# Kernel optimization log

Hardware: AMD Instinct MI355X
Metric: run time of the kernel (lower is better)

Reference implementation:

```python
import jax, jax.numpy as jnp
import numpy as np

# KroneLinear dims (in_a must equal in_b per the source's matmul contraction)
IN_A = 128
IN_B = 128
OUT_A = 128
OUT_B = 128
N = 4096  # batch


def setup_inputs() -> dict:
    key = jax.random.key(0)
    k1, k2, k3, k4 = jax.random.split(key, 4)
    x = jax.random.normal(k1, (N, IN_A * IN_B), dtype=jnp.float32)
    weight_a = jax.random.normal(k2, (OUT_A, IN_A), dtype=jnp.float32) * 0.05
    weight_b = jax.random.normal(k3, (OUT_B, IN_B), dtype=jnp.float32) * 0.05
    bias = jax.random.normal(k4, (OUT_A * OUT_B,), dtype=jnp.float32) * 0.05
    return {"x": x, "weight_a": weight_a, "weight_b": weight_b, "bias": bias}


def reference(x, weight_a, weight_b, bias):
    # vx: view [-1, in_b, in_a] then permute(0,2,1) -> [N, in_a, in_b]
    vx = x.reshape(-1, IN_B, IN_A).transpose(0, 2, 1)
    # torch.matmul(weight_b, vx): contracts weight_b's in_b with vx's dim-1 (in_a)
    # -> [N, out_b, in_b]
    bvx = jnp.einsum('ok,nkj->noj', weight_b, vx)
    # bvx @ weight_a.T -> [N, out_b, out_a]
    bvxa = jnp.einsum('noj,aj->noa', bvx, weight_a)
    # permute(0,2,1) -> [N, out_a, out_b], flatten, add bias
    y = bvxa.transpose(0, 2, 1).reshape(-1, OUT_A * OUT_B) + bias
    return y
```

## Files before the change

### kernel.cpp

```cpp
#include <hip/hip_runtime.h>

typedef __bf16 bf16x8 __attribute__((ext_vector_type(8)));
typedef float f32x4 __attribute__((ext_vector_type(4)));
typedef unsigned int u32x4 __attribute__((ext_vector_type(4)));
typedef unsigned short u16x4 __attribute__((ext_vector_type(4)));

__device__ __forceinline__ unsigned short f2b(float f) {
  union { float f; unsigned int u; } a; a.f = f;
  unsigned int u = a.u;
  u += 0x7fffu + ((u >> 16) & 1u);
  return (unsigned short)(u >> 16);
}

#define LDW 136

__global__ void prep_weights(const float* __restrict__ wa,
                             const float* __restrict__ wb,
                             unsigned short* __restrict__ owa,
                             unsigned short* __restrict__ owb) {
  int t = blockIdx.x * 256 + threadIdx.x;
  if (t < 16384) {
    int j    = t & 7;
    int lane = (t >> 3) & 63;
    int kk   = (t >> 9) & 3;
    int mp   = t >> 11;
    int quad = lane >> 4, l16 = lane & 15;
    owa[t] = f2b(wa[(mp * 16 + l16) * 128 + kk * 32 + quad * 8 + j]);
  } else {
    int u = t - 16384;
    owb[u] = f2b(wb[u]);
  }
}

__global__ __launch_bounds__(512, 4)
void krone_kernel(const float* __restrict__ x,
                  const unsigned short* __restrict__ waf,
                  const unsigned short* __restrict__ wb,
                  const float* __restrict__ bias,
                  float* __restrict__ out) {
  __shared__ unsigned short Mlds[128 * LDW];

  const int tid  = threadIdx.x;
  const int lane = tid & 63;
  const int w    = tid >> 6;
  const int quad = lane >> 4;
  const int l16  = lane & 15;

  const float* xrow = x + (size_t)blockIdx.x * 16384;
  #pragma unroll
  for (int i = 0; i < 8; ++i) {
    int idx = (i << 9) + tid;
    f32x4 v = *(const f32x4*)(xrow + (idx << 2));
    int r = idx >> 5;
    int c = (idx & 31) << 2;
    u16x4 h;
    h[0] = f2b(v[0]); h[1] = f2b(v[1]); h[2] = f2b(v[2]); h[3] = f2b(v[3]);
    *(u16x4*)&Mlds[r * LDW + c] = h;
  }

  bf16x8 wbf[4];
  {
    const unsigned short* wbr = wb + (w * 16 + l16) * 128 + quad * 8;
    #pragma unroll
    for (int kk = 0; kk < 4; ++kk)
      wbf[kk] = __builtin_bit_cast(bf16x8, *(const u32x4*)(wbr + kk * 32));
  }

  __syncthreads();

  u16x4 ur[8];
  #pragma unroll
  for (int m = 0; m < 8; ++m) {
    f32x4 acc = {0.f, 0.f, 0.f, 0.f};
    const unsigned short* mr = &Mlds[(m * 16 + l16) * LDW + quad * 8];
    #pragma unroll
    for (int kk = 0; kk < 4; ++kk) {
      u32x4 ua = *(const u32x4*)(mr + kk * 32);
      acc = __builtin_amdgcn_mfma_f32_16x16x32_bf16(
              __builtin_bit_cast(bf16x8, ua), wbf[kk], acc, 0, 0, 0);
    }
    u16x4 h;
    h[0] = f2b(acc[0]); h[1] = f2b(acc[1]); h[2] = f2b(acc[2]); h[3] = f2b(acc[3]);
    ur[m] = h;
  }

  __syncthreads();

  #pragma unroll
  for (int m = 0; m < 8; ++m)
    *(u16x4*)&Mlds[(w * 16 + l16) * LDW + m * 16 + quad * 4] = ur[m];

  bf16x8 uf[4];
  {
    const unsigned short* utr = &Mlds[(w * 16 + l16) * LDW + quad * 8];
    #pragma unroll
    for (int kk = 0; kk < 4; ++kk)
      uf[kk] = __builtin_bit_cast(bf16x8, *(const u32x4*)(utr + kk * 32));
  }

  float* orow = out + (size_t)blockIdx.x * 16384;
  const unsigned short* wafl = waf + lane * 8;
  #pragma unroll
  for (int mp = 0; mp < 8; ++mp) {
    f32x4 acc = {0.f, 0.f, 0.f, 0.f};
    #pragma unroll
    for (int kk = 0; kk < 4; ++kk) {
      u32x4 ub = *(const u32x4*)(wafl + (mp * 4 + kk) * 512);
      acc = __builtin_amdgcn_mfma_f32_16x16x32_bf16(
              uf[kk], __builtin_bit_cast(bf16x8, ub), acc, 0, 0, 0);
    }
    int r  = mp * 16 + l16;
    int c0 = w * 16 + quad * 4;
    f32x4 b = *(const f32x4*)(bias + r * 128 + c0);
    f32x4 y = acc + b;
    *(f32x4*)(orow + r * 128 + c0) = y;
  }
}

extern "C" void kernel_launch(void* const* d_in, const int* in_sizes, int n_in,
                              void* d_out, int out_size, void* d_ws, size_t ws_size,
                              hipStream_t stream) {
  const float* x  = (const float*)d_in[0];
  const float* wa = (const float*)d_in[1];
  const float* wb = (const float*)d_in[2];
  const float* bs = (const float*)d_in[3];
  float* out = (float*)d_out;

  unsigned short* wsa = (unsigned short*)d_ws;
  unsigned short* wsb = wsa + 128 * 128;

  int N = in_sizes[0] / 16384;

  prep_weights<<<128, 256, 0, stream>>>(wa, wb, wsa, wsb);
  krone_kernel<<<N, 512, 0, stream>>>(x, wsa, wsb, bs, out);
}
```

Baseline: 475.5 us.

## Process four batch rows per block with register-prefetched input pipeline

```diff
diff --git a/kernel.cpp b/kernel.cpp
--- a/kernel.cpp
+++ b/kernel.cpp
@@ -13,6 +13,7 @@
 }
 
 #define LDW 136
+#define G   4
 
 __global__ void prep_weights(const float* __restrict__ wa,
                              const float* __restrict__ wb,
@@ -37,7 +38,7 @@
                   const unsigned short* __restrict__ waf,
                   const unsigned short* __restrict__ wb,
                   const float* __restrict__ bias,
-                  float* __restrict__ out) {
+                  float* __restrict__ out, int Ntot) {
   __shared__ unsigned short Mlds[128 * LDW];
 
   const int tid  = threadIdx.x;
@@ -45,18 +46,11 @@
   const int w    = tid >> 6;
   const int quad = lane >> 4;
   const int l16  = lane & 15;
+  const int n0   = blockIdx.x * G;
+  const int ns   = (Ntot - n0 < G) ? (Ntot - n0) : G;
 
-  const float* xrow = x + (size_t)blockIdx.x * 16384;
-  #pragma unroll
-  for (int i = 0; i < 8; ++i) {
-    int idx = (i << 9) + tid;
-    f32x4 v = *(const f32x4*)(xrow + (idx << 2));
-    int r = idx >> 5;
-    int c = (idx & 31) << 2;
-    u16x4 h;
-    h[0] = f2b(v[0]); h[1] = f2b(v[1]); h[2] = f2b(v[2]); h[3] = f2b(v[3]);
-    *(u16x4*)&Mlds[r * LDW + c] = h;
-  }
+  const int sr = tid >> 5;
+  const int sc = (tid & 31) << 2;
 
   bf16x8 wbf[4];
   {
@@ -66,54 +60,95 @@
       wbf[kk] = __builtin_bit_cast(bf16x8, *(const u32x4*)(wbr + kk * 32));
   }
 
+  f32x4 R[8];
+  {
+    const float* xr = x + (size_t)n0 * 16384 + (tid << 2);
+    #pragma unroll
+    for (int i = 0; i < 8; ++i)
+      R[i] = *(const f32x4*)(xr + (i << 11));
+  }
+  #pragma unroll
+  for (int i = 0; i < 8; ++i) {
+    u16x4 h;
+    h[0] = f2b(R[i][0]); h[1] = f2b(R[i][1]); h[2] = f2b(R[i][2]); h[3] = f2b(R[i][3]);
+    *(u16x4*)&Mlds[(sr + i * 16) * LDW + sc] = h;
+  }
+  if (1 < ns) {
+    const float* xr = x + (size_t)(n0 + 1) * 16384 + (tid << 2);
+    #pragma unroll
+    for (int i = 0; i < 8; ++i)
+      R[i] = *(const f32x4*)(xr + (i << 11));
+  }
   __syncthreads();
 
-  u16x4 ur[8];
-  #pragma unroll
-  for (int m = 0; m < 8; ++m) {
-    f32x4 acc = {0.f, 0.f, 0.f, 0.f};
-    const unsigned short* mr = &Mlds[(m * 16 + l16) * LDW + quad * 8];
+  #pragma unroll 1
+  for (int s = 0; s < ns; ++s) {
+    const int n = n0 + s;
+
+    u16x4 ur[8];
     #pragma unroll
-    for (int kk = 0; kk < 4; ++kk) {
-      u32x4 ua = *(const u32x4*)(mr + kk * 32);
-      acc = __builtin_amdgcn_mfma_f32_16x16x32_bf16(
-              __builtin_bit_cast(bf16x8, ua), wbf[kk], acc, 0, 0, 0);
+    for (int m = 0; m < 8; ++m) {
+      f32x4 acc = {0.f, 0.f, 0.f, 0.f};
+      const unsigned short* mr = &Mlds[(m * 16 + l16) * LDW + quad * 8];
+      #pragma unroll
+      for (int kk = 0; kk < 4; ++kk) {
+        u32x4 ua = *(const u32x4*)(mr + kk * 32);
+        acc = __builtin_amdgcn_mfma_f32_16x16x32_bf16(
+                __builtin_bit_cast(bf16x8, ua), wbf[kk], acc, 0, 0, 0);
+      }
+      u16x4 h;
+      h[0] = f2b(acc[0]); h[1] = f2b(acc[1]); h[2] = f2b(acc[2]); h[3] = f2b(acc[3]);
+      ur[m] = h;
     }
-    u16x4 h;
-    h[0] = f2b(acc[0]); h[1] = f2b(acc[1]); h[2] = f2b(acc[2]); h[3] = f2b(acc[3]);
-    ur[m] = h;
-  }
 
-  __syncthreads();
+    __syncthreads();
 
-  #pragma unroll
-  for (int m = 0; m < 8; ++m)
-    *(u16x4*)&Mlds[(w * 16 + l16) * LDW + m * 16 + quad * 4] = ur[m];
+    #pragma unroll
+    for (int m = 0; m < 8; ++m)
+      *(u16x4*)&Mlds[(w * 16 + l16) * LDW + m * 16 + quad * 4] = ur[m];
+    bf16x8 uf[4];
+    {
+      const unsigned short* utr = &Mlds[(w * 16 + l16) * LDW + quad * 8];
+      #pragma unroll
+      for (int kk = 0; kk < 4; ++kk)
+        uf[kk] = __builtin_bit_cast(bf16x8, *(const u32x4*)(utr + kk * 32));
+    }
 
-  bf16x8 uf[4];
-  {
-    const unsigned short* utr = &Mlds[(w * 16 + l16) * LDW + quad * 8];
+    __syncthreads();
+
+    if (s + 1 < ns) {
+      #pragma unroll
+      for (int i = 0; i < 8; ++i) {
+        u16x4 h;
+        h[0] = f2b(R[i][0]); h[1] = f2b(R[i][1]); h[2] = f2b(R[i][2]); h[3] = f2b(R[i][3]);
+        *(u16x4*)&Mlds[(sr + i * 16) * LDW + sc] = h;
+      }
+      if (s + 2 < ns) {
+        const float* xr = x + (size_t)(n + 2) * 16384 + (tid << 2);
+        #pragma unroll
+        for (int i = 0; i < 8; ++i)
+          R[i] = *(const f32x4*)(xr + (i << 11));
+      }
+    }
+
+    float* orow = out + (size_t)n * 16384;
+    const unsigned short* wafl = waf + lane * 8;
     #pragma unroll
-    for (int kk = 0; kk < 4; ++kk)
-      uf[kk] = __builtin_bit_cast(bf16x8, *(const u32x4*)(utr + kk * 32));
-  }
+    for (int mp = 0; mp < 8; ++mp) {
+      f32x4 acc = {0.f, 0.f, 0.f, 0.f};
+      #pragma unroll
+      for (int kk = 0; kk < 4; ++kk) {
+        u32x4 ub = *(const u32x4*)(wafl + (mp * 4 + kk) * 512);
+        acc = __builtin_amdgcn_mfma_f32_16x16x32_bf16(
+                uf[kk], __builtin_bit_cast(bf16x8, ub), acc, 0, 0, 0);
+      }
+      int r  = mp * 16 + l16;
+      int c0 = w * 16 + quad * 4;
+      f32x4 b = *(const f32x4*)(bias + r * 128 + c0);
+      *(f32x4*)(orow + r * 128 + c0) = acc + b;
+    }
 
-  float* orow = out + (size_t)blockIdx.x * 16384;
-  const unsigned short* wafl = waf + lane * 8;
-  #pragma unroll
-  for (int mp = 0; mp < 8; ++mp) {
-    f32x4 acc = {0.f, 0.f, 0.f, 0.f};
-    #pragma unroll
-    for (int kk = 0; kk < 4; ++kk) {
-      u32x4 ub = *(const u32x4*)(wafl + (mp * 4 + kk) * 512);
-      acc = __builtin_amdgcn_mfma_f32_16x16x32_bf16(
-              uf[kk], __builtin_bit_cast(bf16x8, ub), acc, 0, 0, 0);
-    }
-    int r  = mp * 16 + l16;
-    int c0 = w * 16 + quad * 4;
-    f32x4 b = *(const f32x4*)(bias + r * 128 + c0);
-    f32x4 y = acc + b;
-    *(f32x4*)(orow + r * 128 + c0) = y;
+    __syncthreads();
   }
 }
 
@@ -132,5 +167,6 @@
   int N = in_sizes[0] / 16384;
 
   prep_weights<<<128, 256, 0, stream>>>(wa, wb, wsa, wsb);
-  krone_kernel<<<N, 512, 0, stream>>>(x, wsa, wsb, bs, out);
+  int nblk = (N + G - 1) / G;
+  krone_kernel<<<nblk, 512, 0, stream>>>(x, wsa, wsb, bs, out, N);
 }
```

After: 648.1 us. 1.36x slower.
